# Performance work log

Hardware: AMD Instinct MI355X
Metric: run time of the kernel (lower is better)

## Reference

```python
import jax, jax.numpy as jnp
import numpy as np

PATCH = 3
PAD = PATCH // 2  # stride = 1


def _extract_patches(x):
    """torch F.unfold(k=3, s=1, p=1) reshaped to [b, n=h*w, c*3*3] (c slowest, then ki, kj)."""
    b, c, h, w = x.shape
    xp = jnp.pad(x, ((0, 0), (0, 0), (PAD, PAD), (PAD, PAD)))
    # stack the 9 shifted views -> [b, c, 9, h, w]
    pats = jnp.stack([xp[:, :, i:i + h, j:j + w]
                      for i in range(PATCH) for j in range(PATCH)], axis=2)
    pats = pats.reshape(b, c, PATCH, PATCH, h, w)
    # -> [b, h*w, c*PATCH*PATCH], matching torch unfold channel ordering
    return pats.transpose(0, 4, 5, 1, 2, 3).reshape(b, h * w, c * PATCH * PATCH)


def _l2_normalize(x):
    # F.normalize(dim=2): x / max(||x||_2, 1e-12)
    n = jnp.linalg.norm(x, axis=2, keepdims=True)
    return x / jnp.maximum(n, 1e-12)


def _fold(patches_flat, c, h, w):
    """torch F.fold(k=3, s=1, p=1): overlap-add patches back to [b, c, h, w]."""
    b = patches_flat.shape[0]
    p = patches_flat.reshape(b, h, w, c, PATCH, PATCH)
    out = jnp.zeros((b, c, h + 2 * PAD, w + 2 * PAD), patches_flat.dtype)
    for i in range(PATCH):
        for j in range(PATCH):
            out = out.at[:, :, i:i + h, j:j + w].add(
                p[:, :, :, :, i, j].transpose(0, 3, 1, 2))
    return out[:, :, PAD:PAD + h, PAD:PAD + w]


def setup_inputs() -> dict:
    key = jax.random.key(0)
    k1, k2 = jax.random.split(key)
    B, C, H, W = 1, 256, 96, 96
    return {
        "content_features": jax.random.normal(k1, (B, C, H, W), dtype=jnp.float32),
        "style_features": jax.random.normal(k2, (B, C, H, W), dtype=jnp.float32),
    }


def reference(content_features, style_features):
    b, c, h, w = content_features.shape
    cpat = _extract_patches(content_features)   # [b, n, d]
    spat = _extract_patches(style_features)     # [b, m, d]
    # all-pairs cosine similarity: [b, n, m]
    sim = jnp.einsum('bnd,bmd->bnm', _l2_normalize(cpat), _l2_normalize(spat))
    best = jnp.argmax(sim, axis=2)              # [b, n]
    matched = jnp.take_along_axis(spat, best[:, :, None], axis=1)  # [b, n, d]
    num = _fold(matched, c, h, w)
    den = _fold(jnp.ones_like(matched), c, h, w)
    return num / (den + 1e-8)
```

## Files before the change

kernel.cpp:

```cpp
#include <hip/hip_runtime.h>

#define HH 96
#define WW 96
#define CCH 256
#define NPIX (HH*WW)
#define HP 98
#define NROWS 9604
#define CORE_LO 99
#define CORE_HI 9505
#define CAND_CAP 256

typedef unsigned short u16;
typedef _Float16 f16;
typedef _Float16 f16x8 __attribute__((ext_vector_type(8)));
typedef _Float16 f16x4 __attribute__((ext_vector_type(4)));
typedef float f32x4 __attribute__((ext_vector_type(4)));
typedef int i32x4 __attribute__((ext_vector_type(4)));

__device__ __forceinline__ f32x4 ld4u(const float* p) {
    f32x4 r; __builtin_memcpy(&r, p, 16); return r;
}
__device__ __forceinline__ i32x4 ld4ui(const int* p) {
    i32x4 r; __builtin_memcpy(&r, p, 16); return r;
}
__device__ __forceinline__ float dec_key(unsigned ku) {
    return (ku & 0x80000000u) ? __uint_as_float(ku ^ 0x80000000u)
                              : __uint_as_float(~ku);
}
__device__ __forceinline__ unsigned enc_key(float v) {
    unsigned u = __float_as_uint(v);
    return (u & 0x80000000u) ? ~u : (u | 0x80000000u);
}

__device__ __forceinline__ void stage4(const u16* const* srcs, u16* dst, int kb) {
#pragma unroll
    for (int t = 0; t < 4; ++t)
        __builtin_amdgcn_global_load_lds(
            (const __attribute__((address_space(1))) unsigned int*)(srcs[t] + kb),
            (__attribute__((address_space(3))) unsigned int*)(dst + t * 512),
            16, 0, 0);
}

__global__ __launch_bounds__(256) void xsth_kernel(const float* __restrict__ X,
                                                   float* __restrict__ XT,
                                                   u16* __restrict__ XTh) {
    __shared__ float tile[64][65];
    const int p0 = blockIdx.x * 64, c0 = blockIdx.y * 64;
    const int rr = threadIdx.x >> 6, cl = threadIdx.x & 63;
#pragma unroll
    for (int r = 0; r < 16; ++r)
        tile[rr * 16 + r][cl] = X[(c0 + rr * 16 + r) * NPIX + p0 + cl];
    __syncthreads();
#pragma unroll
    for (int r = 0; r < 16; ++r) {
        float v = tile[cl][rr * 16 + r];
        long long o = (long long)(p0 + rr * 16 + r) * CCH + c0 + cl;
        XT[o] = v;
        f16 h = (f16)v;
        u16 hb; __builtin_memcpy(&hb, &h, 2);
        XTh[o] = hb;
    }
}

__global__ __launch_bounds__(256) void prep_kernel(const float* __restrict__ X,
                                                   float* __restrict__ ssum,
                                                   unsigned long long* __restrict__ keys,
                                                   int* __restrict__ cnt,
                                                   unsigned* __restrict__ dropMax,
                                                   int reset) {
    int p = blockIdx.x * 256 + threadIdx.x;
    if (p >= NPIX) return;
    float s = 0.f;
#pragma unroll 8
    for (int c = 0; c < CCH; ++c) {
        float v = X[c * NPIX + p];
        s = fmaf(v, v, s);
    }
    ssum[p] = s;
    if (reset) { keys[p] = 0ULL; cnt[p] = 0; dropMax[p] = 0u; }
}

__global__ __launch_bounds__(256) void rnsbp_kernel(const float* __restrict__ ssum,
                                                    float* __restrict__ rnsp,
                                                    float* __restrict__ biasp,
                                                    int* __restrict__ midxp) {
    int mp = blockIdx.x * 256 + threadIdx.x;
    if (mp >= 9632) return;
    int yq = mp / HP, xq = mp - yq * HP;
    bool real = (yq >= 1 && yq <= 96 && xq >= 1 && xq <= 96);
    if (!real) { rnsp[mp] = 0.f; biasp[mp] = -3e38f; midxp[mp] = 0; return; }
    int y = yq - 1, x = xq - 1;
    float s = 0.f;
    for (int dy = -1; dy <= 1; ++dy) {
        int yy = y + dy;
        if ((unsigned)yy >= HH) continue;
        for (int dx = -1; dx <= 1; ++dx) {
            int xx = x + dx;
            if ((unsigned)xx >= WW) continue;
            s += ssum[yy * WW + xx];
        }
    }
    rnsp[mp] = 1.f / fmaxf(sqrtf(s), 1e-12f);
    biasp[mp] = 0.f;
    midxp[mp] = y * WW + x;
}

__global__ __launch_bounds__(256) void cthr_kernel(const float* __restrict__ ssum,
                                                   float* __restrict__ thr) {
    int n = blockIdx.x * 256 + threadIdx.x;
    if (n >= NPIX) return;
    int y = n / WW, x = n - y * WW;
    float s = 0.f;
    for (int dy = -1; dy <= 1; ++dy) {
        int yy = y + dy;
        if ((unsigned)yy >= HH) continue;
        for (int dx = -1; dx <= 1; ++dx) {
            int xx = x + dx;
            if ((unsigned)xx >= WW) continue;
            s += ssum[yy * WW + xx];
        }
    }
    thr[n] = 0.0036f * sqrtf(s);
}

__global__ __launch_bounds__(256) void padzero_kernel(u16* __restrict__ cc, int wstride) {
    int p = blockIdx.x;
    int yq = p / HP, xq = p - yq * HP;
    if (yq >= 1 && yq <= 96 && xq >= 1 && xq <= 96) return;
    const f32x4 z = {0.f, 0.f, 0.f, 0.f};
    u16* row = cc + (long long)p * wstride;
    for (int c = threadIdx.x * 8; c < wstride; c += 2048)
        *(f32x4*)&row[c] = z;
}

__global__ __launch_bounds__(256, 4) void cc_gemm_kernel(
        const u16* __restrict__ ChT, const u16* __restrict__ ShT,
        const u16* __restrict__ zbuf,
        u16* __restrict__ cc, int csp, int wstride) {
    __shared__ u16 lds[2][2][8][64][8];

    const int tid = threadIdx.x;
    const int n0 = blockIdx.x * 128;
    const int m0 = blockIdx.y * 128;
    const int wave = tid >> 6, lane = tid & 63;
    const int wr = wave >> 1, wc = wave & 1;
    const int rlo = lane & 15, kseg = (lane >> 4) * 8;
    const int isB = wave >> 1;
    const int tb = (wave & 1) * 4;

    const u16* srcs[4];
    if (!isB) {
#pragma unroll
        for (int t = 0; t < 4; ++t)
            srcs[t] = ChT + (n0 + (tb + t) * 16 + rlo) * CCH + kseg;
    } else {
#pragma unroll
        for (int t = 0; t < 4; ++t) {
            int qp = csp + m0 + (tb + t) * 16 + rlo;
            int yq = qp / HP, xq = qp - yq * HP;
            bool ok = (qp < NROWS) && (yq >= 1 && yq <= 96 && xq >= 1 && xq <= 96);
            srcs[t] = ok ? (ShT + ((yq - 1) * WW + (xq - 1)) * CCH + kseg)
                         : (zbuf + kseg);
        }
    }
    u16* slab0 = &lds[0][isB][tb][0][0];
    u16* slab1 = &lds[1][isB][tb][0][0];

    f32x4 acc[4][4];
#pragma unroll
    for (int i = 0; i < 4; ++i)
#pragma unroll
        for (int j = 0; j < 4; ++j) acc[i][j] = (f32x4){0.f, 0.f, 0.f, 0.f};

    stage4(srcs, slab0, 0);
    stage4(srcs, slab1, 32);

#define READS(CUR)                                                          \
    f16x8 ah[4], bh[4];                                                     \
    _Pragma("unroll")                                                       \
    for (int i = 0; i < 4; ++i) {                                           \
        ah[i] = *(const f16x8*)&lds[CUR][0][wr * 4 + i][lane][0];           \
        bh[i] = *(const f16x8*)&lds[CUR][1][wc * 4 + i][lane][0];           \
    }

#define MFMAS                                                               \
    _Pragma("unroll")                                                       \
    for (int i = 0; i < 4; ++i)                                             \
        _Pragma("unroll")                                                   \
        for (int j = 0; j < 4; ++j)                                         \
            acc[i][j] = __builtin_amdgcn_mfma_f32_16x16x32_f16(ah[i], bh[j], acc[i][j], 0, 0, 0);

#define KSTEP(KK, WN)                                                       \
    {                                                                       \
        asm volatile("s_waitcnt vmcnt(" #WN ")" ::: "memory");              \
        __builtin_amdgcn_sched_barrier(0);                                  \
        __builtin_amdgcn_s_barrier();                                       \
        READS((KK) & 1)                                                     \
        asm volatile("s_waitcnt lgkmcnt(0)" ::: "memory");                  \
        __builtin_amdgcn_sched_barrier(0);                                  \
        __builtin_amdgcn_s_barrier();                                       \
        if ((KK) + 2 < 8)                                                   \
            stage4(srcs, (((KK) & 1)) ? slab1 : slab0, ((KK) + 2) * 32);    \
        __builtin_amdgcn_sched_barrier(0);                                  \
        MFMAS                                                               \
    }

    KSTEP(0, 4) KSTEP(1, 4) KSTEP(2, 4) KSTEP(3, 4)
    KSTEP(4, 4) KSTEP(5, 4) KSTEP(6, 4) KSTEP(7, 0)

#undef KSTEP
#undef MFMAS
#undef READS

    const int r0 = (lane >> 4) * 4;
    const int cl = lane & 15;
#pragma unroll
    for (int i = 0; i < 4; ++i) {
        const int prow = n0 + wr * 64 + i * 16 + r0;
#pragma unroll
        for (int r = 0; r < 4; ++r) {
            const int row = prow + r;
            const int pp = row + 2 * (row / WW) + CORE_LO;
            const long long base = (long long)pp * wstride + m0 + wc * 64 + cl;
#pragma unroll
            for (int j = 0; j < 4; ++j) {
                f16 h = (f16)acc[i][j][r];
                u16 hb; __builtin_memcpy(&hb, &h, 2);
                cc[base + j * 16] = hb;
            }
        }
    }
}

__global__ __launch_bounds__(256) void boxsum_kernel(
        const u16* __restrict__ cc, const float* __restrict__ rnsp,
        const float* __restrict__ biasp, const int* __restrict__ midxp,
        const float* __restrict__ thr,
        unsigned long long* __restrict__ keys,
        int* __restrict__ cnt, float* __restrict__ candV, u16* __restrict__ candI,
        unsigned* __restrict__ dropMax,
        int core0, int coreEnd, int csp, int wstride) {
    const int wave = threadIdx.x >> 6, lane = threadIdx.x & 63;
    const int nb = (blockIdx.x & 7) * (NPIX / 32) + (blockIdx.x >> 3);
    const int n = nb * 4 + wave;
    const int pp = n + 2 * (n / WW) + CORE_LO;
    const int W1 = wstride + 1;
    const float thrn = thr[n];

    float wmax = -1e30f;
    {
        unsigned long long k0 = keys[n];
        if (k0) wmax = dec_key((unsigned)(k0 >> 32));
    }

    const int ODD[6] = {-99, -97, -1, 1, 97, 99};
    const int EVN[3] = {-98, 0, 98};
    const long long B0 = (long long)pp * wstride + (core0 + lane * 4 - csp);
    const u16* po[6]; const u16* pe[3];
#pragma unroll
    for (int t = 0; t < 6; ++t) po[t] = cc + B0 + (long long)ODD[t] * W1;
#pragma unroll
    for (int t = 0; t < 3; ++t) pe[t] = cc + B0 + (long long)EVN[t] * W1 - 1;

    for (int mq = core0 + lane * 4; mq < coreEnd; mq += 256) {
        f32x4 s = {0.f, 0.f, 0.f, 0.f};
#pragma unroll
        for (int t = 0; t < 6; ++t) {
            f16x4 a; __builtin_memcpy(&a, po[t], 8); po[t] += 256;
            s[0] += (float)a[0]; s[1] += (float)a[1];
            s[2] += (float)a[2]; s[3] += (float)a[3];
        }
#pragma unroll
        for (int t = 0; t < 3; ++t) {
            f16x8 a; __builtin_memcpy(&a, pe[t], 16); pe[t] += 256;
            s[0] += (float)a[1]; s[1] += (float)a[2];
            s[2] += (float)a[3]; s[3] += (float)a[4];
        }
        f32x4 rv = ld4u(rnsp + mq);
        f32x4 bv = ld4u(biasp + mq);
        i32x4 iv = ld4ui(midxp + mq);
        float v[4];
#pragma unroll
        for (int sl = 0; sl < 4; ++sl) {
            v[sl] = fmaf(s[sl], rv[sl], bv[sl]);
            if (mq + sl >= coreEnd) v[sl] = -3e38f;
        }
        float im = fmaxf(fmaxf(v[0], v[1]), fmaxf(v[2], v[3]));
#pragma unroll
        for (int d = 32; d; d >>= 1) im = fmaxf(im, __shfl_xor(im, d));
        wmax = fmaxf(wmax, im);
#pragma unroll
        for (int sl = 0; sl < 4; ++sl) {
            if (v[sl] >= wmax - thrn) {
                int idx = atomicAdd(&cnt[n], 1);
                if (idx < CAND_CAP) {
                    candV[n * CAND_CAP + idx] = v[sl];
                    candI[n * CAND_CAP + idx] = (u16)iv[sl];
                } else {
                    atomicMax(&dropMax[n], enc_key(v[sl]));
                }
            }
        }
    }
    if (lane == 0)
        atomicMax(&keys[n], ((unsigned long long)enc_key(wmax)) << 32);
}

__global__ __launch_bounds__(256) void rescore_kernel(
        const float* __restrict__ XcT, const float* __restrict__ XsT,
        const float* __restrict__ rnsp, const float* __restrict__ thr,
        const unsigned long long* __restrict__ keys,
        const int* __restrict__ cnt, const float* __restrict__ candV,
        const u16* __restrict__ candI, const unsigned* __restrict__ dropMax,
        int* __restrict__ bestm) {
    const int wave = threadIdx.x >> 6, lane = threadIdx.x & 63;
    const int n = blockIdx.x * 4 + wave;
    int c = cnt[n]; if (c > CAND_CAP) c = CAND_CAP;
    const float M = dec_key((unsigned)(keys[n] >> 32));
    const float lim = M - thr[n];

    unsigned dm = dropMax[n];
    bool fallback = dm && (dec_key(dm) >= lim);
    if (!fallback) {
        int npass = 0, lastk = -1;
        for (int k = 0; k < c; ++k) {
            if (candV[n * CAND_CAP + k] >= lim) { ++npass; if (lastk < 0) lastk = k; }
        }
        if (npass == 1) {
            if (lane == 0) bestm[n] = candI[n * CAND_CAP + lastk];
            return;
        }
    }

    const int yn = n / WW, xn = n - yn * WW;
    const f32x4 z = {0.f, 0.f, 0.f, 0.f};
    f32x4 an[9];
#pragma unroll
    for (int t = 0; t < 9; ++t) {
        int di = t / 3 - 1, dj = t % 3 - 1;
        bool ok = ((unsigned)(yn + di) < HH) && ((unsigned)(xn + dj) < WW);
        an[t] = ok ? ld4u(XcT + (long long)((yn + di) * WW + xn + dj) * CCH + lane * 4) : z;
    }
    float bv = -1e30f; int bm = 0x7fffffff;
    if (fallback) {
        for (int m = 0; m < NPIX; ++m) {
            int ym = m / WW, xm = m - ym * WW;
            f32x4 acc = z;
#pragma unroll
            for (int t = 0; t < 9; ++t) {
                int di = t / 3 - 1, dj = t % 3 - 1;
                if (((unsigned)(ym + di) < HH) && ((unsigned)(xm + dj) < WW))
                    acc += an[t] * ld4u(XsT + (long long)((ym + di) * WW + xm + dj) * CCH + lane * 4);
            }
            float d = acc[0] + acc[1] + acc[2] + acc[3];
#pragma unroll
            for (int dd = 32; dd; dd >>= 1) d += __shfl_xor(d, dd);
            float v = d * rnsp[(ym + 1) * HP + (xm + 1)];
            if (v > bv) { bv = v; bm = m; }
        }
    } else {
        for (int k = 0; k < c; ++k) {
            if (candV[n * CAND_CAP + k] < lim) continue;
            int m = candI[n * CAND_CAP + k];
            int ym = m / WW, xm = m - ym * WW;
            f32x4 acc = z;
#pragma unroll
            for (int t = 0; t < 9; ++t) {
                int di = t / 3 - 1, dj = t % 3 - 1;
                if (((unsigned)(ym + di) < HH) && ((unsigned)(xm + dj) < WW))
                    acc += an[t] * ld4u(XsT + (long long)((ym + di) * WW + xm + dj) * CCH + lane * 4);
            }
            float d = acc[0] + acc[1] + acc[2] + acc[3];
#pragma unroll
            for (int dd = 32; dd; dd >>= 1) d += __shfl_xor(d, dd);
            float v = d * rnsp[(ym + 1) * HP + (xm + 1)];
            if (v > bv || (v == bv && m < bm)) { bv = v; bm = m; }
        }
    }
    if (lane == 0) bestm[n] = bm;
}

__global__ __launch_bounds__(256) void fold2_kernel(const float* __restrict__ XsT,
                                                    const int* __restrict__ bestm,
                                                    float* __restrict__ outT) {
    const int wave = threadIdx.x >> 6, lane = threadIdx.x & 63;
    const int p = blockIdx.x * 4 + wave;
    const int y = p / WW, x = p - y * WW;
    f32x4 num = {0.f, 0.f, 0.f, 0.f};
    int den = 0;
#pragma unroll
    for (int i = 0; i < 3; ++i) {
        int ny = y + 1 - i;
        if ((unsigned)ny >= HH) continue;
#pragma unroll
        for (int j = 0; j < 3; ++j) {
            int nx = x + 1 - j;
            if ((unsigned)nx >= WW) continue;
            den++;
            int mg = bestm[ny * WW + nx];
            int my = mg / WW, mx = mg - my * WW;
            int sy = my + i - 1, sx = mx + j - 1;
            if ((unsigned)sy < HH && (unsigned)sx < WW)
                num += ld4u(XsT + (long long)(sy * WW + sx) * CCH + lane * 4);
        }
    }
    float inv = 1.f / ((float)den + 1e-8f);
    f32x4 o = {num[0] * inv, num[1] * inv, num[2] * inv, num[3] * inv};
    *(f32x4*)&outT[(long long)p * CCH + lane * 4] = o;
}

__global__ __launch_bounds__(256) void outtr_kernel(const float* __restrict__ outT,
                                                    float* __restrict__ out) {
    __shared__ float tile[64][65];
    const int p0 = blockIdx.x * 64, c0 = blockIdx.y * 64;
    const int t = threadIdx.x;
    const int rr = t >> 6, cl = t & 63;
#pragma unroll
    for (int r = 0; r < 16; ++r)
        tile[rr * 16 + r][cl] = outT[(long long)(p0 + rr * 16 + r) * CCH + c0 + cl];
    __syncthreads();
#pragma unroll
    for (int r = 0; r < 16; ++r)
        out[(long long)(c0 + rr * 16 + r) * NPIX + p0 + cl] = tile[cl][rr * 16 + r];
}

extern "C" void kernel_launch(void* const* d_in, const int* in_sizes, int n_in,
                              void* d_out, int out_size, void* d_ws, size_t ws_size,
                              hipStream_t stream) {
    (void)in_sizes; (void)n_in; (void)out_size;
    const float* Xc = (const float*)d_in[0];
    const float* Xs = (const float*)d_in[1];
    float* out = (float*)d_out;

    char* w = (char*)d_ws;
    unsigned long long* keys = (unsigned long long*)w;  w += (size_t)NPIX * 8;
    float* XcT  = (float*)w;                            w += (size_t)NPIX * CCH * 4;
    float* XsT  = (float*)w;                            w += (size_t)NPIX * CCH * 4;
    float* outT = (float*)w;                            w += (size_t)NPIX * CCH * 4;
    u16* XcH = (u16*)w;                                 w += (size_t)NPIX * CCH * 2;
    u16* XsH = (u16*)w;                                 w += (size_t)NPIX * CCH * 2;
    float* ssum_s = (float*)w;                          w += (size_t)NPIX * 4;
    float* ssum_c = (float*)w;                          w += (size_t)NPIX * 4;
    float* rnsp  = (float*)w;                           w += (size_t)9632 * 4;
    float* biasp = (float*)w;                           w += (size_t)9632 * 4;
    int*   midxp = (int*)w;                             w += (size_t)9632 * 4;
    float* thr   = (float*)w;                           w += (size_t)NPIX * 4;
    int*   cnt   = (int*)w;                             w += (size_t)NPIX * 4;
    int*   bestm = (int*)w;                             w += (size_t)NPIX * 4;
    unsigned* dropMax = (unsigned*)w;                   w += (size_t)NPIX * 4;
    float* candV = (float*)w;                           w += (size_t)NPIX * CAND_CAP * 4;
    u16*   candI = (u16*)w;                             w += (size_t)NPIX * CAND_CAP * 2;
    u16*   zbuf  = (u16*)w;                             w += 1024;
    u16*   ccbuf = (u16*)w;
    const size_t fixed = (size_t)(w - (char*)d_ws);

    long long avail = (ws_size > fixed + 4096)
                        ? (long long)(ws_size - fixed - 4096) : 0;
    int wstride = (int)(((avail / ((long long)NROWS * 2)) / 128) * 128);
    if (wstride > 4992) wstride = 4992;
    if (wstride < 512) wstride = 512;
    const int McCore = wstride - 198;

    hipMemsetAsync(zbuf, 0, 1024, stream);
    dim3 gt(NPIX / 64, CCH / 64);
    xsth_kernel<<<gt, 256, 0, stream>>>(Xc, XcT, XcH);
    xsth_kernel<<<gt, 256, 0, stream>>>(Xs, XsT, XsH);
    prep_kernel<<<NPIX / 256, 256, 0, stream>>>(Xs, ssum_s, keys, cnt, dropMax, 1);
    prep_kernel<<<NPIX / 256, 256, 0, stream>>>(Xc, ssum_c, keys, cnt, dropMax, 0);
    rnsbp_kernel<<<38, 256, 0, stream>>>(ssum_s, rnsp, biasp, midxp);
    cthr_kernel<<<NPIX / 256, 256, 0, stream>>>(ssum_c, thr);
    padzero_kernel<<<NROWS, 256, 0, stream>>>(ccbuf, wstride);

    for (int core0 = CORE_LO; core0 < CORE_HI; core0 += McCore) {
        int coreEnd = (core0 + McCore < CORE_HI) ? core0 + McCore : CORE_HI;
        int csp = core0 - 99;
        int ce = coreEnd + 99; if (ce > NROWS) ce = NROWS;
        int Wc = ce - csp;
        dim3 g(NPIX / 128, (Wc + 127) / 128);
        cc_gemm_kernel<<<g, 256, 0, stream>>>(XcH, XsH, zbuf, ccbuf, csp, wstride);
        boxsum_kernel<<<NPIX / 4, 256, 0, stream>>>(ccbuf, rnsp, biasp, midxp, thr,
                                                    keys, cnt, candV, candI, dropMax,
                                                    core0, coreEnd, csp, wstride);
    }

    rescore_kernel<<<NPIX / 4, 256, 0, stream>>>(XcT, XsT, rnsp, thr, keys,
                                                 cnt, candV, candI, dropMax, bestm);
    fold2_kernel<<<NPIX / 4, 256, 0, stream>>>(XsT, bestm, outT);
    outtr_kernel<<<gt, 256, 0, stream>>>(outT, out);
}
```

Baseline: 462.3 us.

## Split boxsum into max pass and candidate-emission pass with final threshold

Restructures the boxsum kernel into two sweeps over the fp16 similarity tile. The first computes each row's full maximum, and the second recomputes the box sums and emits candidates only against the final threshold. Previously candidates were filtered against a running max, so early iterations could admit many spurious candidates and atomics. The change also removes the per-iteration wave shuffle reduction, drops the blockIdx swizzle, and unrolls the loops by two, at the cost of reading the tile twice.

```diff
diff --git a/kernel.cpp b/kernel.cpp
--- a/kernel.cpp
+++ b/kernel.cpp
@@ -241,8 +241,7 @@
         unsigned* __restrict__ dropMax,
         int core0, int coreEnd, int csp, int wstride) {
     const int wave = threadIdx.x >> 6, lane = threadIdx.x & 63;
-    const int nb = (blockIdx.x & 7) * (NPIX / 32) + (blockIdx.x >> 3);
-    const int n = nb * 4 + wave;
+    const int n = blockIdx.x * 4 + wave;
     const int pp = n + 2 * (n / WW) + CORE_LO;
     const int W1 = wstride + 1;
     const float thrn = thr[n];
@@ -256,48 +255,77 @@
     const int ODD[6] = {-99, -97, -1, 1, 97, 99};
     const int EVN[3] = {-98, 0, 98};
     const long long B0 = (long long)pp * wstride + (core0 + lane * 4 - csp);
-    const u16* po[6]; const u16* pe[3];
-#pragma unroll
-    for (int t = 0; t < 6; ++t) po[t] = cc + B0 + (long long)ODD[t] * W1;
-#pragma unroll
-    for (int t = 0; t < 3; ++t) pe[t] = cc + B0 + (long long)EVN[t] * W1 - 1;
-
-    for (int mq = core0 + lane * 4; mq < coreEnd; mq += 256) {
-        f32x4 s = {0.f, 0.f, 0.f, 0.f};
-#pragma unroll
-        for (int t = 0; t < 6; ++t) {
-            f16x4 a; __builtin_memcpy(&a, po[t], 8); po[t] += 256;
-            s[0] += (float)a[0]; s[1] += (float)a[1];
-            s[2] += (float)a[2]; s[3] += (float)a[3];
-        }
-#pragma unroll
-        for (int t = 0; t < 3; ++t) {
-            f16x8 a; __builtin_memcpy(&a, pe[t], 16); pe[t] += 256;
-            s[0] += (float)a[1]; s[1] += (float)a[2];
-            s[2] += (float)a[3]; s[3] += (float)a[4];
-        }
-        f32x4 rv = ld4u(rnsp + mq);
-        f32x4 bv = ld4u(biasp + mq);
-        i32x4 iv = ld4ui(midxp + mq);
-        float v[4];
-#pragma unroll
-        for (int sl = 0; sl < 4; ++sl) {
-            v[sl] = fmaf(s[sl], rv[sl], bv[sl]);
-            if (mq + sl >= coreEnd) v[sl] = -3e38f;
-        }
-        float im = fmaxf(fmaxf(v[0], v[1]), fmaxf(v[2], v[3]));
-#pragma unroll
-        for (int d = 32; d; d >>= 1) im = fmaxf(im, __shfl_xor(im, d));
-        wmax = fmaxf(wmax, im);
-#pragma unroll
-        for (int sl = 0; sl < 4; ++sl) {
-            if (v[sl] >= wmax - thrn) {
-                int idx = atomicAdd(&cnt[n], 1);
-                if (idx < CAND_CAP) {
-                    candV[n * CAND_CAP + idx] = v[sl];
-                    candI[n * CAND_CAP + idx] = (u16)iv[sl];
-                } else {
-                    atomicMax(&dropMax[n], enc_key(v[sl]));
+
+    float lmax = -3e38f;
+    {
+        const u16* po[6]; const u16* pe[3];
+#pragma unroll
+        for (int t = 0; t < 6; ++t) po[t] = cc + B0 + (long long)ODD[t] * W1;
+#pragma unroll
+        for (int t = 0; t < 3; ++t) pe[t] = cc + B0 + (long long)EVN[t] * W1 - 1;
+#pragma unroll 2
+        for (int mq = core0 + lane * 4; mq < coreEnd; mq += 256) {
+            f32x4 s = {0.f, 0.f, 0.f, 0.f};
+#pragma unroll
+            for (int t = 0; t < 6; ++t) {
+                f16x4 a; __builtin_memcpy(&a, po[t], 8); po[t] += 256;
+                s[0] += (float)a[0]; s[1] += (float)a[1];
+                s[2] += (float)a[2]; s[3] += (float)a[3];
+            }
+#pragma unroll
+            for (int t = 0; t < 3; ++t) {
+                f16x8 a; __builtin_memcpy(&a, pe[t], 16); pe[t] += 256;
+                s[0] += (float)a[1]; s[1] += (float)a[2];
+                s[2] += (float)a[3]; s[3] += (float)a[4];
+            }
+            f32x4 rv = ld4u(rnsp + mq);
+            f32x4 bv = ld4u(biasp + mq);
+#pragma unroll
+            for (int sl = 0; sl < 4; ++sl) {
+                float v = fmaf(s[sl], rv[sl], bv[sl]);
+                if (mq + sl < coreEnd) lmax = fmaxf(lmax, v);
+            }
+        }
+    }
+#pragma unroll
+    for (int d = 32; d; d >>= 1) lmax = fmaxf(lmax, __shfl_xor(lmax, d));
+    wmax = fmaxf(wmax, lmax);
+    const float lim = wmax - thrn;
+
+    {
+        const u16* po[6]; const u16* pe[3];
+#pragma unroll
+        for (int t = 0; t < 6; ++t) po[t] = cc + B0 + (long long)ODD[t] * W1;
+#pragma unroll
+        for (int t = 0; t < 3; ++t) pe[t] = cc + B0 + (long long)EVN[t] * W1 - 1;
+#pragma unroll 2
+        for (int mq = core0 + lane * 4; mq < coreEnd; mq += 256) {
+            f32x4 s = {0.f, 0.f, 0.f, 0.f};
+#pragma unroll
+            for (int t = 0; t < 6; ++t) {
+                f16x4 a; __builtin_memcpy(&a, po[t], 8); po[t] += 256;
+                s[0] += (float)a[0]; s[1] += (float)a[1];
+                s[2] += (float)a[2]; s[3] += (float)a[3];
+            }
+#pragma unroll
+            for (int t = 0; t < 3; ++t) {
+                f16x8 a; __builtin_memcpy(&a, pe[t], 16); pe[t] += 256;
+                s[0] += (float)a[1]; s[1] += (float)a[2];
+                s[2] += (float)a[3]; s[3] += (float)a[4];
+            }
+            f32x4 rv = ld4u(rnsp + mq);
+            f32x4 bv = ld4u(biasp + mq);
+#pragma unroll
+            for (int sl = 0; sl < 4; ++sl) {
+                float v = fmaf(s[sl], rv[sl], bv[sl]);
+                if (mq + sl < coreEnd && v >= lim) {
+                    int idx = atomicAdd(&cnt[n], 1);
+                    if (idx < CAND_CAP) {
+                        candV[n * CAND_CAP + idx] = v;
+                        candI[n * CAND_CAP + idx] = (u16)midxp[mq + sl];
+                    } else {
+                        atomicMax(&dropMax[n], enc_key(v));
+                    }
                 }
             }
         }
```

Measured after the change: 544.5 us. 1.18x slower.

## Store channel-correlation buffer in fp32 and use top-2 candidate selection in boxsum

Applied to the files above, without the earlier changes.

The correlation GEMM output is stored as fp32 instead of fp16, which doubles the buffer size and halves the maximum chunk width (wstride capped at 2560), so more GEMM and boxsum chunk iterations are needed. The boxsum kernel now keeps a per-lane top-2 during a single pass. It emits candidates only after a wave-wide max is known and rescans the row only when the second-best value passes the threshold, which cuts atomics and emitted candidates. It also drops the midx lookup table in favour of computing indices, and removes the block-index swizzle.

```diff
diff --git a/kernel.cpp b/kernel.cpp
--- a/kernel.cpp
+++ b/kernel.cpp
@@ -13,15 +13,10 @@
 typedef unsigned short u16;
 typedef _Float16 f16;
 typedef _Float16 f16x8 __attribute__((ext_vector_type(8)));
-typedef _Float16 f16x4 __attribute__((ext_vector_type(4)));
 typedef float f32x4 __attribute__((ext_vector_type(4)));
-typedef int i32x4 __attribute__((ext_vector_type(4)));
 
 __device__ __forceinline__ f32x4 ld4u(const float* p) {
     f32x4 r; __builtin_memcpy(&r, p, 16); return r;
-}
-__device__ __forceinline__ i32x4 ld4ui(const int* p) {
-    i32x4 r; __builtin_memcpy(&r, p, 16); return r;
 }
 __device__ __forceinline__ float dec_key(unsigned ku) {
     return (ku & 0x80000000u) ? __uint_as_float(ku ^ 0x80000000u)
@@ -30,6 +25,10 @@
 __device__ __forceinline__ unsigned enc_key(float v) {
     unsigned u = __float_as_uint(v);
     return (u & 0x80000000u) ? ~u : (u | 0x80000000u);
+}
+__device__ __forceinline__ int pad2m(int mp) {
+    int yq = mp / HP, xq = mp - yq * HP;
+    return (yq - 1) * WW + (xq - 1);
 }
 
 __device__ __forceinline__ void stage4(const u16* const* srcs, u16* dst, int kb) {
@@ -82,13 +81,12 @@
 
 __global__ __launch_bounds__(256) void rnsbp_kernel(const float* __restrict__ ssum,
                                                     float* __restrict__ rnsp,
-                                                    float* __restrict__ biasp,
-                                                    int* __restrict__ midxp) {
+                                                    float* __restrict__ biasp) {
     int mp = blockIdx.x * 256 + threadIdx.x;
     if (mp >= 9632) return;
     int yq = mp / HP, xq = mp - yq * HP;
     bool real = (yq >= 1 && yq <= 96 && xq >= 1 && xq <= 96);
-    if (!real) { rnsp[mp] = 0.f; biasp[mp] = -3e38f; midxp[mp] = 0; return; }
+    if (!real) { rnsp[mp] = 0.f; biasp[mp] = -3e38f; return; }
     int y = yq - 1, x = xq - 1;
     float s = 0.f;
     for (int dy = -1; dy <= 1; ++dy) {
@@ -102,7 +100,6 @@
     }
     rnsp[mp] = 1.f / fmaxf(sqrtf(s), 1e-12f);
     biasp[mp] = 0.f;
-    midxp[mp] = y * WW + x;
 }
 
 __global__ __launch_bounds__(256) void cthr_kernel(const float* __restrict__ ssum,
@@ -123,20 +120,20 @@
     thr[n] = 0.0036f * sqrtf(s);
 }
 
-__global__ __launch_bounds__(256) void padzero_kernel(u16* __restrict__ cc, int wstride) {
+__global__ __launch_bounds__(256) void padzero_kernel(float* __restrict__ cc, int wstride) {
     int p = blockIdx.x;
     int yq = p / HP, xq = p - yq * HP;
     if (yq >= 1 && yq <= 96 && xq >= 1 && xq <= 96) return;
     const f32x4 z = {0.f, 0.f, 0.f, 0.f};
-    u16* row = cc + (long long)p * wstride;
-    for (int c = threadIdx.x * 8; c < wstride; c += 2048)
+    float* row = cc + (long long)p * wstride;
+    for (int c = threadIdx.x * 4; c < wstride; c += 1024)
         *(f32x4*)&row[c] = z;
 }
 
 __global__ __launch_bounds__(256, 4) void cc_gemm_kernel(
         const u16* __restrict__ ChT, const u16* __restrict__ ShT,
         const u16* __restrict__ zbuf,
-        u16* __restrict__ cc, int csp, int wstride) {
+        float* __restrict__ cc, int csp, int wstride) {
     __shared__ u16 lds[2][2][8][64][8];
 
     const int tid = threadIdx.x;
@@ -223,81 +220,92 @@
             const int pp = row + 2 * (row / WW) + CORE_LO;
             const long long base = (long long)pp * wstride + m0 + wc * 64 + cl;
 #pragma unroll
-            for (int j = 0; j < 4; ++j) {
-                f16 h = (f16)acc[i][j][r];
-                u16 hb; __builtin_memcpy(&hb, &h, 2);
-                cc[base + j * 16] = hb;
-            }
+            for (int j = 0; j < 4; ++j)
+                cc[base + j * 16] = acc[i][j][r];
         }
     }
 }
 
 __global__ __launch_bounds__(256) void boxsum_kernel(
-        const u16* __restrict__ cc, const float* __restrict__ rnsp,
-        const float* __restrict__ biasp, const int* __restrict__ midxp,
-        const float* __restrict__ thr,
+        const float* __restrict__ cc, const float* __restrict__ rnsp,
+        const float* __restrict__ biasp, const float* __restrict__ thr,
         unsigned long long* __restrict__ keys,
         int* __restrict__ cnt, float* __restrict__ candV, u16* __restrict__ candI,
         unsigned* __restrict__ dropMax,
         int core0, int coreEnd, int csp, int wstride) {
     const int wave = threadIdx.x >> 6, lane = threadIdx.x & 63;
-    const int nb = (blockIdx.x & 7) * (NPIX / 32) + (blockIdx.x >> 3);
-    const int n = nb * 4 + wave;
+    const int n = blockIdx.x * 4 + wave;
     const int pp = n + 2 * (n / WW) + CORE_LO;
+    const long long rowbase = (long long)pp * wstride - csp;
     const int W1 = wstride + 1;
     const float thrn = thr[n];
 
-    float wmax = -1e30f;
+    float wprior = -1e30f;
     {
         unsigned long long k0 = keys[n];
-        if (k0) wmax = dec_key((unsigned)(k0 >> 32));
-    }
-
-    const int ODD[6] = {-99, -97, -1, 1, 97, 99};
-    const int EVN[3] = {-98, 0, 98};
-    const long long B0 = (long long)pp * wstride + (core0 + lane * 4 - csp);
-    const u16* po[6]; const u16* pe[3];
-#pragma unroll
-    for (int t = 0; t < 6; ++t) po[t] = cc + B0 + (long long)ODD[t] * W1;
-#pragma unroll
-    for (int t = 0; t < 3; ++t) pe[t] = cc + B0 + (long long)EVN[t] * W1 - 1;
-
+        if (k0) wprior = dec_key((unsigned)(k0 >> 32));
+    }
+
+    const int OFF[9] = {-99, -98, -97, -1, 0, 1, 97, 98, 99};
+    const float* tp[9];
+#pragma unroll
+    for (int t = 0; t < 9; ++t)
+        tp[t] = cc + rowbase + core0 + lane * 4 + (long long)OFF[t] * W1;
+
+    float v1 = -3e38f, v2 = -3e38f;
+    int i1 = 0;
     for (int mq = core0 + lane * 4; mq < coreEnd; mq += 256) {
         f32x4 s = {0.f, 0.f, 0.f, 0.f};
 #pragma unroll
-        for (int t = 0; t < 6; ++t) {
-            f16x4 a; __builtin_memcpy(&a, po[t], 8); po[t] += 256;
-            s[0] += (float)a[0]; s[1] += (float)a[1];
-            s[2] += (float)a[2]; s[3] += (float)a[3];
-        }
-#pragma unroll
-        for (int t = 0; t < 3; ++t) {
-            f16x8 a; __builtin_memcpy(&a, pe[t], 16); pe[t] += 256;
-            s[0] += (float)a[1]; s[1] += (float)a[2];
-            s[2] += (float)a[3]; s[3] += (float)a[4];
-        }
+        for (int t = 0; t < 9; ++t) { s += ld4u(tp[t]); tp[t] += 256; }
         f32x4 rv = ld4u(rnsp + mq);
         f32x4 bv = ld4u(biasp + mq);
-        i32x4 iv = ld4ui(midxp + mq);
-        float v[4];
 #pragma unroll
         for (int sl = 0; sl < 4; ++sl) {
-            v[sl] = fmaf(s[sl], rv[sl], bv[sl]);
-            if (mq + sl >= coreEnd) v[sl] = -3e38f;
-        }
-        float im = fmaxf(fmaxf(v[0], v[1]), fmaxf(v[2], v[3]));
-#pragma unroll
-        for (int d = 32; d; d >>= 1) im = fmaxf(im, __shfl_xor(im, d));
-        wmax = fmaxf(wmax, im);
-#pragma unroll
-        for (int sl = 0; sl < 4; ++sl) {
-            if (v[sl] >= wmax - thrn) {
-                int idx = atomicAdd(&cnt[n], 1);
-                if (idx < CAND_CAP) {
-                    candV[n * CAND_CAP + idx] = v[sl];
-                    candI[n * CAND_CAP + idx] = (u16)iv[sl];
-                } else {
-                    atomicMax(&dropMax[n], enc_key(v[sl]));
+            float v = fmaf(s[sl], rv[sl], bv[sl]);
+            if (mq + sl >= coreEnd) v = -3e38f;
+            if (v > v1) { v2 = v1; v1 = v; i1 = mq + sl; }
+            else if (v > v2) v2 = v;
+        }
+    }
+
+    float wmax = v1;
+#pragma unroll
+    for (int d = 32; d; d >>= 1) wmax = fmaxf(wmax, __shfl_xor(wmax, d));
+    wmax = fmaxf(wmax, wprior);
+    const float lim = wmax - thrn;
+
+    if (v1 >= lim) {
+        int idx = atomicAdd(&cnt[n], 1);
+        if (idx < CAND_CAP) {
+            candV[n * CAND_CAP + idx] = v1;
+            candI[n * CAND_CAP + idx] = (u16)pad2m(i1);
+        } else {
+            atomicMax(&dropMax[n], enc_key(v1));
+        }
+    }
+    if (v2 >= lim) {
+        const float* rp[9];
+#pragma unroll
+        for (int t = 0; t < 9; ++t)
+            rp[t] = cc + rowbase + core0 + lane * 4 + (long long)OFF[t] * W1;
+        for (int mq = core0 + lane * 4; mq < coreEnd; mq += 256) {
+            f32x4 s = {0.f, 0.f, 0.f, 0.f};
+#pragma unroll
+            for (int t = 0; t < 9; ++t) { s += ld4u(rp[t]); rp[t] += 256; }
+            f32x4 rv = ld4u(rnsp + mq);
+            f32x4 bv = ld4u(biasp + mq);
+#pragma unroll
+            for (int sl = 0; sl < 4; ++sl) {
+                float v = fmaf(s[sl], rv[sl], bv[sl]);
+                if (mq + sl < coreEnd && v >= lim && (mq + sl) != i1) {
+                    int idx = atomicAdd(&cnt[n], 1);
+                    if (idx < CAND_CAP) {
+                        candV[n * CAND_CAP + idx] = v;
+                        candI[n * CAND_CAP + idx] = (u16)pad2m(mq + sl);
+                    } else {
+                        atomicMax(&dropMax[n], enc_key(v));
+                    }
                 }
             }
         }
@@ -443,7 +451,6 @@
     float* ssum_c = (float*)w;                          w += (size_t)NPIX * 4;
     float* rnsp  = (float*)w;                           w += (size_t)9632 * 4;
     float* biasp = (float*)w;                           w += (size_t)9632 * 4;
-    int*   midxp = (int*)w;                             w += (size_t)9632 * 4;
     float* thr   = (float*)w;                           w += (size_t)NPIX * 4;
     int*   cnt   = (int*)w;                             w += (size_t)NPIX * 4;
     int*   bestm = (int*)w;                             w += (size_t)NPIX * 4;
@@ -451,13 +458,13 @@
     float* candV = (float*)w;                           w += (size_t)NPIX * CAND_CAP * 4;
     u16*   candI = (u16*)w;                             w += (size_t)NPIX * CAND_CAP * 2;
     u16*   zbuf  = (u16*)w;                             w += 1024;
-    u16*   ccbuf = (u16*)w;
+    float* ccbuf = (float*)w;
     const size_t fixed = (size_t)(w - (char*)d_ws);
 
     long long avail = (ws_size > fixed + 4096)
                         ? (long long)(ws_size - fixed - 4096) : 0;
-    int wstride = (int)(((avail / ((long long)NROWS * 2)) / 128) * 128);
-    if (wstride > 4992) wstride = 4992;
+    int wstride = (int)(((avail / ((long long)NROWS * 4)) / 128) * 128);
+    if (wstride > 2560) wstride = 2560;
     if (wstride < 512) wstride = 512;
     const int McCore = wstride - 198;
 
@@ -467,7 +474,7 @@
     xsth_kernel<<<gt, 256, 0, stream>>>(Xs, XsT, XsH);
     prep_kernel<<<NPIX / 256, 256, 0, stream>>>(Xs, ssum_s, keys, cnt, dropMax, 1);
     prep_kernel<<<NPIX / 256, 256, 0, stream>>>(Xc, ssum_c, keys, cnt, dropMax, 0);
-    rnsbp_kernel<<<38, 256, 0, stream>>>(ssum_s, rnsp, biasp, midxp);
+    rnsbp_kernel<<<38, 256, 0, stream>>>(ssum_s, rnsp, biasp);
     cthr_kernel<<<NPIX / 256, 256, 0, stream>>>(ssum_c, thr);
     padzero_kernel<<<NROWS, 256, 0, stream>>>(ccbuf, wstride);
 
@@ -478,7 +485,7 @@
         int Wc = ce - csp;
         dim3 g(NPIX / 128, (Wc + 127) / 128);
         cc_gemm_kernel<<<g, 256, 0, stream>>>(XcH, XsH, zbuf, ccbuf, csp, wstride);
-        boxsum_kernel<<<NPIX / 4, 256, 0, stream>>>(ccbuf, rnsp, biasp, midxp, thr,
+        boxsum_kernel<<<NPIX / 4, 256, 0, stream>>>(ccbuf, rnsp, biasp, thr,
                                                     keys, cnt, candV, candI, dropMax,
                                                     core0, coreEnd, csp, wstride);
     }
```

New measurement: 416.5 us (median of 2 runs). 9.9% less time.
